# Optimization experiments

Measured on AMD Instinct MI355X. Metric: run time of the kernel, lower is better.

The kernel has to match this reference:

```python
import jax, jax.numpy as jnp
import numpy as np

TEMPERATURE = 1.0        # sample_codebook_temperature
COMMITMENT_COST = 1.0

B, T, D, K = 8, 4096, 64, 1024


def setup_inputs() -> dict:
    key = jax.random.key(0)
    k1, k2 = jax.random.split(key)
    x = jax.random.normal(k1, (B, T, D), dtype=jnp.float32)
    embeddings = jax.random.normal(k2, (D, K), dtype=jnp.float32)  # (embedding_dim, codebook_size)
    return {"x": x, "embeddings": embeddings}


def gumbel_softmax(logits, temperature):
    # logits: [N, K]
    K_ = logits.shape[1]
    indices = jnp.argmax(logits, axis=1)
    enc = jax.nn.one_hot(indices, K_, dtype=logits.dtype)
    pi0 = jax.nn.softmax(logits, axis=-1)
    pi1 = (enc + jax.nn.softmax(logits / temperature, axis=-1)) / 2
    pi1 = jax.nn.softmax(jax.lax.stop_gradient(jnp.log(pi1) - logits), axis=1)
    pi2 = 2 * pi1 - 0.5 * pi0
    encodings = pi2 - jax.lax.stop_gradient(pi2) + enc  # straight-through encodings
    return indices, encodings


def reference(x, embeddings):
    D_, K_ = embeddings.shape
    flat = x.reshape(-1, D_)                              # [N, D]
    # squared euclidean distances via matmul (cdist trick)
    sim = flat @ embeddings                               # [N, K]
    dist = (jnp.sum(flat ** 2, axis=1, keepdims=True)
            - 2.0 * sim
            + jnp.sum(embeddings ** 2, axis=0, keepdims=True))
    indices, encodings = gumbel_softmax(-dist, TEMPERATURE)
    indices = indices.reshape(x.shape[:-1])               # [B, T]
    quantized = embeddings.T[indices]                     # gather: [B, T, D]
    e_latent_loss = jnp.mean(jnp.square(jax.lax.stop_gradient(quantized) - x))
    loss = e_latent_loss * COMMITMENT_COST
    # straight-through estimator (training-mode output; same values as eval)
    quantized = x + jax.lax.stop_gradient(quantized - x)
    return quantized, encodings, indices, loss
```

## Files before the change

kernel.cpp:

```cpp
#include <hip/hip_runtime.h>
#include <hip/hip_bf16.h>


#define NROWS 32768
#define DDIM  64
#define KCB   1024
#define MARGIN 0.02f

typedef float    f32x4 __attribute__((ext_vector_type(4)));
typedef _Float16 f16x8 __attribute__((ext_vector_type(8)));

#define WS_ET    0
#define WS_H     65536
#define WS_PART  66560
#define WS_EHI   68608
#define WS_ELO   101376

__global__ __launch_bounds__(64) void kA_prep(const float* __restrict__ E,
                                              float* __restrict__ Et,
                                              float* __restrict__ h,
                                              _Float16* __restrict__ Ehi,
                                              _Float16* __restrict__ Elo) {
  int k = blockIdx.x * 64 + threadIdx.x;
  float col[DDIM];
  float sum = 0.f;
#pragma unroll
  for (int d = 0; d < DDIM; ++d) {
    float v = E[d * KCB + k];
    col[d] = v;
    sum = fmaf(v, v, sum);
  }
  float4* dst = (float4*)(Et + (size_t)k * DDIM);
#pragma unroll
  for (int i = 0; i < 16; ++i)
    dst[i] = make_float4(col[4*i], col[4*i+1], col[4*i+2], col[4*i+3]);
  h[k] = 0.5f * sum;

#pragma unroll
  for (int w = 0; w < 2; ++w) {
    f16x8 hi8[4], lo8[4];
#pragma unroll
    for (int p = 0; p < 32; ++p) {
      int dl = w * 32 + 4 * (p >> 3) + (p & 3) + 16 * ((p >> 2) & 1);
      float v = col[dl];
      _Float16 hi = (_Float16)v;
      hi8[p >> 3][p & 7] = hi;
      lo8[p >> 3][p & 7] = (_Float16)(v - (float)hi);
    }
#pragma unroll
    for (int q = 0; q < 4; ++q) {
      *(f16x8*)(Ehi + (size_t)k * DDIM + w * 32 + q * 8) = hi8[q];
      *(f16x8*)(Elo + (size_t)k * DDIM + w * 32 + q * 8) = lo8[q];
    }
  }
}

__global__ __launch_bounds__(256, 4) void kB_main(const float* __restrict__ x,
                                                  const _Float16* __restrict__ Ehi,
                                                  const _Float16* __restrict__ Elo,
                                                  const float* __restrict__ Et,
                                                  const float* __restrict__ h,
                                                  float* __restrict__ partial,
                                                  float* __restrict__ out_q,
                                                  float* __restrict__ out_enc,
                                                  float* __restrict__ out_ind) {
  __shared__ float mb1[4][16], mb2[4][16];
  __shared__ int   mi1[4][16];
  __shared__ int   sidx[16];
  __shared__ int   flags[16];
  __shared__ int   nflag;
  __shared__ float rbw[4];
  __shared__ int   riw[4];
  __shared__ float red[4];

  int tid  = threadIdx.x;
  int wq   = tid >> 6;
  int lane = tid & 63;
  int g = lane >> 4, c = lane & 15;
  int r0 = blockIdx.x * 16;

  if (tid == 0) nflag = 0;

  f16x8 Ahi[2], Alo[2];
  {
    const float* xb = x + (size_t)(r0 + c) * DDIM;
#pragma unroll
    for (int w = 0; w < 2; ++w) {
      f32x4 xa = *(const f32x4*)(xb + w * 32 + 4 * g);
      f32x4 xc = *(const f32x4*)(xb + w * 32 + 16 + 4 * g);
#pragma unroll
      for (int e = 0; e < 4; ++e) {
        _Float16 hi = (_Float16)xa[e];
        Ahi[w][e] = hi;
        Alo[w][e] = (_Float16)(xa[e] - (float)hi);
      }
#pragma unroll
      for (int e = 0; e < 4; ++e) {
        _Float16 hi = (_Float16)xc[e];
        Ahi[w][4 + e] = hi;
        Alo[w][4 + e] = (_Float16)(xc[e] - (float)hi);
      }
    }
  }

  float b1[4], b2[4];
  int   i1[4];
#pragma unroll
  for (int q = 0; q < 4; ++q) { b1[q] = -3.0e38f; b2[q] = -3.0e38f; i1[q] = 0; }

  const _Float16* peh = Ehi + (size_t)(wq * 256 + c) * DDIM + g * 8;
  const _Float16* pel = Elo + (size_t)(wq * 256 + c) * DDIM + g * 8;

  f16x8 bh0n = *(const f16x8*)(peh);
  f16x8 bl0n = *(const f16x8*)(pel);
  f16x8 bh1n = *(const f16x8*)(peh + 32);
  f16x8 bl1n = *(const f16x8*)(pel + 32);
  float hn = h[wq * 256 + c];

#pragma unroll 1
  for (int ch = 0; ch < 16; ++ch) {
    f16x8 bh0 = bh0n, bl0 = bl0n, bh1 = bh1n, bl1 = bl1n;
    float hc = hn;
    if (ch < 15) {
      size_t off = (size_t)(ch + 1) * 16 * DDIM;
      bh0n = *(const f16x8*)(peh + off);
      bl0n = *(const f16x8*)(pel + off);
      bh1n = *(const f16x8*)(peh + off + 32);
      bl1n = *(const f16x8*)(pel + off + 32);
      hn = h[wq * 256 + (ch + 1) * 16 + c];
    }
    int code = wq * 256 + ch * 16 + c;
    f32x4 a = { -hc, -hc, -hc, -hc };
    a = __builtin_amdgcn_mfma_f32_16x16x32_f16(Alo[0], bh0, a, 0, 0, 0);
    a = __builtin_amdgcn_mfma_f32_16x16x32_f16(Ahi[0], bl0, a, 0, 0, 0);
    a = __builtin_amdgcn_mfma_f32_16x16x32_f16(Ahi[0], bh0, a, 0, 0, 0);
    a = __builtin_amdgcn_mfma_f32_16x16x32_f16(Alo[1], bh1, a, 0, 0, 0);
    a = __builtin_amdgcn_mfma_f32_16x16x32_f16(Ahi[1], bl1, a, 0, 0, 0);
    a = __builtin_amdgcn_mfma_f32_16x16x32_f16(Ahi[1], bh1, a, 0, 0, 0);
#pragma unroll
    for (int q = 0; q < 4; ++q) {
      float s = a[q];
      bool gt = s > b1[q];
      b2[q] = gt ? b1[q] : fmaxf(b2[q], s);
      i1[q] = gt ? code : i1[q];
      b1[q] = gt ? s : b1[q];
    }
  }

#pragma unroll
  for (int step = 1; step <= 8; step <<= 1) {
#pragma unroll
    for (int q = 0; q < 4; ++q) {
      float ob1 = __shfl_xor(b1[q], step);
      int   oi1 = __shfl_xor(i1[q], step);
      float ob2 = __shfl_xor(b2[q], step);
      bool win = (ob1 > b1[q]) || (ob1 == b1[q] && oi1 < i1[q]);
      float loser = win ? b1[q] : ob1;
      b1[q] = win ? ob1 : b1[q];
      i1[q] = win ? oi1 : i1[q];
      b2[q] = fmaxf(fmaxf(b2[q], ob2), loser);
    }
  }
  if (c == 0) {
#pragma unroll
    for (int q = 0; q < 4; ++q) {
      int row = 4 * g + q;
      mb1[wq][row] = b1[q];
      mi1[wq][row] = i1[q];
      mb2[wq][row] = b2[q];
    }
  }
  __syncthreads();

  if (tid < 16) {
    float bb1 = mb1[0][tid], bb2 = mb2[0][tid];
    int   ii1 = mi1[0][tid];
#pragma unroll
    for (int qd = 1; qd < 4; ++qd) {
      float a1 = mb1[qd][tid];
      int   j1 = mi1[qd][tid];
      bool w1 = (a1 > bb1) || (a1 == bb1 && j1 < ii1);
      bb2 = fmaxf(fmaxf(bb2, mb2[qd][tid]), w1 ? bb1 : a1);
      bb1 = w1 ? a1 : bb1;
      ii1 = w1 ? j1 : ii1;
    }
    sidx[tid] = ii1;
    if (bb1 - bb2 <= MARGIN) { int p = atomicAdd(&nflag, 1); flags[p] = tid; }
  }
  __syncthreads();

  int nf = nflag;
#pragma unroll 1
  for (int fi = 0; fi < nf; ++fi) {
    int row = flags[fi];
    int n = r0 + row;
    const f32x4* xr = (const f32x4*)(x + (size_t)n * DDIM);
    float best = -3.0e38f; int bi = 0;
#pragma unroll 1
    for (int j = 0; j < 4; ++j) {
      int code = j * 256 + tid;
      const f32x4* er = (const f32x4*)(Et + (size_t)code * DDIM);
      float acc = -h[code];
#pragma unroll
      for (int d = 0; d < 16; ++d) {
        f32x4 e4 = er[d], x4 = xr[d];
        acc = fmaf(x4[0], e4[0], acc); acc = fmaf(x4[1], e4[1], acc);
        acc = fmaf(x4[2], e4[2], acc); acc = fmaf(x4[3], e4[3], acc);
      }
      if (acc > best || (acc == best && code < bi)) { best = acc; bi = code; }
    }
#pragma unroll
    for (int step = 1; step <= 32; step <<= 1) {
      float ob = __shfl_xor(best, step);
      int   oi = __shfl_xor(bi, step);
      if (ob > best || (ob == best && oi < bi)) { best = ob; bi = oi; }
    }
    if (lane == 0) { rbw[wq] = best; riw[wq] = bi; }
    __syncthreads();
    if (tid == 0) {
      float bb = rbw[0]; int ii = riw[0];
#pragma unroll
      for (int qd = 1; qd < 4; ++qd) {
        bool w1 = (rbw[qd] > bb) || (rbw[qd] == bb && riw[qd] < ii);
        bb = w1 ? rbw[qd] : bb;
        ii = w1 ? riw[qd] : ii;
      }
      sidx[row] = ii;
    }
    __syncthreads();
  }

  if (tid < 16) out_ind[r0 + tid] = (float)sidx[tid];

  float lsum;
  {
    int row = tid >> 4, cc = tid & 15;
    int n = r0 + row;
    int bi = sidx[row];
    f32x4 q4 = *(const f32x4*)(Et + (size_t)bi * DDIM + cc * 4);
    f32x4 x4 = *(const f32x4*)(x + (size_t)n * DDIM + cc * 4);
    float d0 = q4[0] - x4[0], d1 = q4[1] - x4[1], d2 = q4[2] - x4[2], d3 = q4[3] - x4[3];
    lsum = d0 * d0;
    lsum = fmaf(d1, d1, lsum); lsum = fmaf(d2, d2, lsum); lsum = fmaf(d3, d3, lsum);
    *(f32x4*)(out_q + (size_t)n * DDIM + cc * 4) = q4;
  }

#pragma unroll 1
  for (int rr = 0; rr < 16; ++rr) {
    int bk = sidx[rr];
    f32x4 v = (f32x4)(0.f);
    if ((bk >> 2) == tid) v[bk & 3] = 1.0f;
    *(f32x4*)(out_enc + (size_t)(r0 + rr) * KCB + tid * 4) = v;
  }

#pragma unroll
  for (int off = 32; off > 0; off >>= 1) lsum += __shfl_down(lsum, off);
  if (lane == 0) red[wq] = lsum;
  __syncthreads();
  if (tid == 0) partial[blockIdx.x] = red[0] + red[1] + red[2] + red[3];
}

__global__ void k5_loss(const float* __restrict__ partial, float* __restrict__ out_loss) {
  int t = threadIdx.x;
  float s = 0.f;
#pragma unroll
  for (int i = 0; i < 8; ++i) s += partial[t + i * 256];
#pragma unroll
  for (int off = 32; off > 0; off >>= 1) s += __shfl_down(s, off);
  __shared__ float red[4];
  int lane = t & 63, w = t >> 6;
  if (lane == 0) red[w] = s;
  __syncthreads();
  if (t == 0) out_loss[0] = (red[0] + red[1] + red[2] + red[3]) * (1.0f / 2097152.0f);
}

extern "C" void kernel_launch(void* const* d_in, const int* in_sizes, int n_in,
                              void* d_out, int out_size, void* d_ws, size_t ws_size,
                              hipStream_t stream) {
  const float* x = (const float*)d_in[0];
  const float* E = (const float*)d_in[1];

  float* ws   = (float*)d_ws;
  float* Et   = ws + WS_ET;
  float* h    = ws + WS_H;
  float* part = ws + WS_PART;
  _Float16* Ehi = (_Float16*)(ws + WS_EHI);
  _Float16* Elo = (_Float16*)(ws + WS_ELO);

  float* out      = (float*)d_out;
  float* out_q    = out;
  float* out_enc  = out + 2097152;
  float* out_ind  = out + 35651584;
  float* out_loss = out + 35684352;

  kA_prep<<<16, 64, 0, stream>>>(E, Et, h, Ehi, Elo);
  kB_main<<<2048, 256, 0, stream>>>(x, Ehi, Elo, Et, h, part, out_q, out_enc, out_ind);
  k5_loss<<<1, 256, 0, stream>>>(part, out_loss);
}
```

Baseline: 234.0 us.

## Split main kernel into zero-fill, scoring and finalize passes; score 32 rows per block

The one-hot encoding output is now cleared by a dedicated streaming zero-fill kernel, and the finalize kernel only scatters a single 1.0 per row. The scoring kernel handles 32 rows per block, so each codebook fragment loaded is reused across two MFMA row groups, halving codebook traffic per row. Best indices go through a workspace buffer to a separate finalize kernel that writes quantized output, indices and loss partials. This adds two launches and an extra pass over the encoding buffer's write ordering, and the register count in the scoring kernel grows.

```diff
diff --git a/kernel.cpp b/kernel.cpp
--- a/kernel.cpp
+++ b/kernel.cpp
@@ -13,8 +13,9 @@
 #define WS_ET    0
 #define WS_H     65536
 #define WS_PART  66560
-#define WS_EHI   68608
-#define WS_ELO   101376
+#define WS_IBEST 68608
+#define WS_EHI   101376
+#define WS_ELO   134144
 
 __global__ __launch_bounds__(64) void kA_prep(const float* __restrict__ E,
                                               float* __restrict__ Et,
@@ -55,35 +56,41 @@
   }
 }
 
-__global__ __launch_bounds__(256, 4) void kB_main(const float* __restrict__ x,
-                                                  const _Float16* __restrict__ Ehi,
-                                                  const _Float16* __restrict__ Elo,
-                                                  const float* __restrict__ Et,
-                                                  const float* __restrict__ h,
-                                                  float* __restrict__ partial,
-                                                  float* __restrict__ out_q,
-                                                  float* __restrict__ out_enc,
-                                                  float* __restrict__ out_ind) {
-  __shared__ float mb1[4][16], mb2[4][16];
-  __shared__ int   mi1[4][16];
-  __shared__ int   sidx[16];
-  __shared__ int   flags[16];
+__global__ __launch_bounds__(256) void kZ_zero(float* __restrict__ out_enc) {
+  size_t t = (size_t)blockIdx.x * 256 + threadIdx.x;
+  f32x4* p = (f32x4*)out_enc;
+  f32x4 z = (f32x4)(0.f);
+#pragma unroll
+  for (int i = 0; i < 16; ++i)
+    p[t + (size_t)i * 524288] = z;
+}
+
+__global__ __launch_bounds__(256, 4) void kB_score(const float* __restrict__ x,
+                                                   const _Float16* __restrict__ Ehi,
+                                                   const _Float16* __restrict__ Elo,
+                                                   const float* __restrict__ Et,
+                                                   const float* __restrict__ h,
+                                                   int* __restrict__ ibest) {
+  __shared__ float mb1[4][32], mb2[4][32];
+  __shared__ int   mi1[4][32];
+  __shared__ int   sidx[32];
+  __shared__ int   flags[32];
   __shared__ int   nflag;
   __shared__ float rbw[4];
   __shared__ int   riw[4];
-  __shared__ float red[4];
 
   int tid  = threadIdx.x;
   int wq   = tid >> 6;
   int lane = tid & 63;
   int g = lane >> 4, c = lane & 15;
-  int r0 = blockIdx.x * 16;
+  int r0 = blockIdx.x * 32;
 
   if (tid == 0) nflag = 0;
 
-  f16x8 Ahi[2], Alo[2];
-  {
-    const float* xb = x + (size_t)(r0 + c) * DDIM;
+  f16x8 Ahi[2][2], Alo[2][2];
+#pragma unroll
+  for (int rg = 0; rg < 2; ++rg) {
+    const float* xb = x + (size_t)(r0 + rg * 16 + c) * DDIM;
 #pragma unroll
     for (int w = 0; w < 2; ++w) {
       f32x4 xa = *(const f32x4*)(xb + w * 32 + 4 * g);
@@ -91,22 +98,24 @@
 #pragma unroll
       for (int e = 0; e < 4; ++e) {
         _Float16 hi = (_Float16)xa[e];
-        Ahi[w][e] = hi;
-        Alo[w][e] = (_Float16)(xa[e] - (float)hi);
+        Ahi[rg][w][e] = hi;
+        Alo[rg][w][e] = (_Float16)(xa[e] - (float)hi);
       }
 #pragma unroll
       for (int e = 0; e < 4; ++e) {
         _Float16 hi = (_Float16)xc[e];
-        Ahi[w][4 + e] = hi;
-        Alo[w][4 + e] = (_Float16)(xc[e] - (float)hi);
-      }
-    }
-  }
-
-  float b1[4], b2[4];
-  int   i1[4];
-#pragma unroll
-  for (int q = 0; q < 4; ++q) { b1[q] = -3.0e38f; b2[q] = -3.0e38f; i1[q] = 0; }
+        Ahi[rg][w][4 + e] = hi;
+        Alo[rg][w][4 + e] = (_Float16)(xc[e] - (float)hi);
+      }
+    }
+  }
+
+  float b1[2][4], b2[2][4];
+  int   i1[2][4];
+#pragma unroll
+  for (int rg = 0; rg < 2; ++rg)
+#pragma unroll
+    for (int q = 0; q < 4; ++q) { b1[rg][q] = -3.0e38f; b2[rg][q] = -3.0e38f; i1[rg][q] = 0; }
 
   const _Float16* peh = Ehi + (size_t)(wq * 256 + c) * DDIM + g * 8;
   const _Float16* pel = Elo + (size_t)(wq * 256 + c) * DDIM + g * 8;
@@ -130,49 +139,56 @@
       hn = h[wq * 256 + (ch + 1) * 16 + c];
     }
     int code = wq * 256 + ch * 16 + c;
-    f32x4 a = { -hc, -hc, -hc, -hc };
-    a = __builtin_amdgcn_mfma_f32_16x16x32_f16(Alo[0], bh0, a, 0, 0, 0);
-    a = __builtin_amdgcn_mfma_f32_16x16x32_f16(Ahi[0], bl0, a, 0, 0, 0);
-    a = __builtin_amdgcn_mfma_f32_16x16x32_f16(Ahi[0], bh0, a, 0, 0, 0);
-    a = __builtin_amdgcn_mfma_f32_16x16x32_f16(Alo[1], bh1, a, 0, 0, 0);
-    a = __builtin_amdgcn_mfma_f32_16x16x32_f16(Ahi[1], bl1, a, 0, 0, 0);
-    a = __builtin_amdgcn_mfma_f32_16x16x32_f16(Ahi[1], bh1, a, 0, 0, 0);
-#pragma unroll
-    for (int q = 0; q < 4; ++q) {
-      float s = a[q];
-      bool gt = s > b1[q];
-      b2[q] = gt ? b1[q] : fmaxf(b2[q], s);
-      i1[q] = gt ? code : i1[q];
-      b1[q] = gt ? s : b1[q];
+#pragma unroll
+    for (int rg = 0; rg < 2; ++rg) {
+      f32x4 a = { -hc, -hc, -hc, -hc };
+      a = __builtin_amdgcn_mfma_f32_16x16x32_f16(Alo[rg][0], bh0, a, 0, 0, 0);
+      a = __builtin_amdgcn_mfma_f32_16x16x32_f16(Ahi[rg][0], bl0, a, 0, 0, 0);
+      a = __builtin_amdgcn_mfma_f32_16x16x32_f16(Ahi[rg][0], bh0, a, 0, 0, 0);
+      a = __builtin_amdgcn_mfma_f32_16x16x32_f16(Alo[rg][1], bh1, a, 0, 0, 0);
+      a = __builtin_amdgcn_mfma_f32_16x16x32_f16(Ahi[rg][1], bl1, a, 0, 0, 0);
+      a = __builtin_amdgcn_mfma_f32_16x16x32_f16(Ahi[rg][1], bh1, a, 0, 0, 0);
+#pragma unroll
+      for (int q = 0; q < 4; ++q) {
+        float s = a[q];
+        bool gt = s > b1[rg][q];
+        b2[rg][q] = gt ? b1[rg][q] : fmaxf(b2[rg][q], s);
+        i1[rg][q] = gt ? code : i1[rg][q];
+        b1[rg][q] = gt ? s : b1[rg][q];
+      }
     }
   }
 
 #pragma unroll
   for (int step = 1; step <= 8; step <<= 1) {
 #pragma unroll
-    for (int q = 0; q < 4; ++q) {
-      float ob1 = __shfl_xor(b1[q], step);
-      int   oi1 = __shfl_xor(i1[q], step);
-      float ob2 = __shfl_xor(b2[q], step);
-      bool win = (ob1 > b1[q]) || (ob1 == b1[q] && oi1 < i1[q]);
-      float loser = win ? b1[q] : ob1;
-      b1[q] = win ? ob1 : b1[q];
-      i1[q] = win ? oi1 : i1[q];
-      b2[q] = fmaxf(fmaxf(b2[q], ob2), loser);
-    }
+    for (int rg = 0; rg < 2; ++rg)
+#pragma unroll
+      for (int q = 0; q < 4; ++q) {
+        float ob1 = __shfl_xor(b1[rg][q], step);
+        int   oi1 = __shfl_xor(i1[rg][q], step);
+        float ob2 = __shfl_xor(b2[rg][q], step);
+        bool win = (ob1 > b1[rg][q]) || (ob1 == b1[rg][q] && oi1 < i1[rg][q]);
+        float loser = win ? b1[rg][q] : ob1;
+        b1[rg][q] = win ? ob1 : b1[rg][q];
+        i1[rg][q] = win ? oi1 : i1[rg][q];
+        b2[rg][q] = fmaxf(fmaxf(b2[rg][q], ob2), loser);
+      }
   }
   if (c == 0) {
 #pragma unroll
-    for (int q = 0; q < 4; ++q) {
-      int row = 4 * g + q;
-      mb1[wq][row] = b1[q];
-      mi1[wq][row] = i1[q];
-      mb2[wq][row] = b2[q];
-    }
-  }
-  __syncthreads();
-
-  if (tid < 16) {
+    for (int rg = 0; rg < 2; ++rg)
+#pragma unroll
+      for (int q = 0; q < 4; ++q) {
+        int row = rg * 16 + 4 * g + q;
+        mb1[wq][row] = b1[rg][q];
+        mi1[wq][row] = i1[rg][q];
+        mb2[wq][row] = b2[rg][q];
+      }
+  }
+  __syncthreads();
+
+  if (tid < 32) {
     float bb1 = mb1[0][tid], bb2 = mb2[0][tid];
     int   ii1 = mi1[0][tid];
 #pragma unroll
@@ -230,7 +246,28 @@
     __syncthreads();
   }
 
-  if (tid < 16) out_ind[r0 + tid] = (float)sidx[tid];
+  if (tid < 32) ibest[r0 + tid] = sidx[tid];
+}
+
+__global__ __launch_bounds__(256) void kC_fin(const float* __restrict__ x,
+                                              const float* __restrict__ Et,
+                                              const int* __restrict__ ibest,
+                                              float* __restrict__ partial,
+                                              float* __restrict__ out_q,
+                                              float* __restrict__ out_enc,
+                                              float* __restrict__ out_ind) {
+  __shared__ int sidx[16];
+  int tid = threadIdx.x;
+  int r0 = blockIdx.x * 16;
+
+  if (tid < 16) {
+    int n = r0 + tid;
+    int bi = ibest[n];
+    sidx[tid] = bi;
+    out_ind[n] = (float)bi;
+    out_enc[(size_t)n * KCB + bi] = 1.0f;
+  }
+  __syncthreads();
 
   float lsum;
   {
@@ -245,17 +282,11 @@
     *(f32x4*)(out_q + (size_t)n * DDIM + cc * 4) = q4;
   }
 
-#pragma unroll 1
-  for (int rr = 0; rr < 16; ++rr) {
-    int bk = sidx[rr];
-    f32x4 v = (f32x4)(0.f);
-    if ((bk >> 2) == tid) v[bk & 3] = 1.0f;
-    *(f32x4*)(out_enc + (size_t)(r0 + rr) * KCB + tid * 4) = v;
-  }
-
 #pragma unroll
   for (int off = 32; off > 0; off >>= 1) lsum += __shfl_down(lsum, off);
-  if (lane == 0) red[wq] = lsum;
+  __shared__ float red[4];
+  int lane = tid & 63, w = tid >> 6;
+  if (lane == 0) red[w] = lsum;
   __syncthreads();
   if (tid == 0) partial[blockIdx.x] = red[0] + red[1] + red[2] + red[3];
 }
@@ -284,6 +315,7 @@
   float* Et   = ws + WS_ET;
   float* h    = ws + WS_H;
   float* part = ws + WS_PART;
+  int*   ibest = (int*)(ws + WS_IBEST);
   _Float16* Ehi = (_Float16*)(ws + WS_EHI);
   _Float16* Elo = (_Float16*)(ws + WS_ELO);
 
@@ -294,6 +326,8 @@
   float* out_loss = out + 35684352;
 
   kA_prep<<<16, 64, 0, stream>>>(E, Et, h, Ehi, Elo);
-  kB_main<<<2048, 256, 0, stream>>>(x, Ehi, Elo, Et, h, part, out_q, out_enc, out_ind);
+  kZ_zero<<<2048, 256, 0, stream>>>(out_enc);
+  kB_score<<<1024, 256, 0, stream>>>(x, Ehi, Elo, Et, h, ibest);
+  kC_fin<<<2048, 256, 0, stream>>>(x, Et, ibest, part, out_q, out_enc, out_ind);
   k5_loss<<<1, 256, 0, stream>>>(part, out_loss);
 }
```

Measured after the change: 233.9 us. About the same (-0.1%).
